# Kernel tuning notes

Measured on AMD Instinct MI355X. Metric: run time of the kernel, lower is better.

The kernel has to match this reference:

```python
import jax, jax.numpy as jnp
import numpy as np

DIVERSITY_RATE = 0.5


def setup_inputs() -> dict:
    key = jax.random.key(0)
    k1, k2 = jax.random.split(key)
    # model log-probabilities at current step: (bsz, beam, vocab)
    lprobs = jax.nn.log_softmax(
        jax.random.normal(k1, (128, 5, 50257), dtype=jnp.float32), axis=-1
    )
    # historical hypothesis scores: (bsz, beam, step)
    scores = jax.random.normal(k2, (128, 5, 10), dtype=jnp.float32)
    return {"lprobs": lprobs, "scores": scores, "step": 10}


def reference(lprobs, scores, step):
    bsz, beam_size, vocab_size = lprobs.shape
    k = min(beam_size * 2, beam_size * vocab_size - 1)  # = 10 here

    # step > 0 path: accumulate running score of each hypothesis
    lp = lprobs + scores[:, :, step - 1][:, :, None]  # (bsz, beam, vocab)

    # 1/ per-beam top-k over vocab (vectorized over all beams at once)
    s, idx = jax.lax.top_k(lp, k)  # (bsz, beam, k); idx already < vocab (fmod no-op)

    # 2/,3/ intra-sibling ordering -> rank penalty (rank r gets r*rate)
    sibling_score = jnp.arange(1, k + 1, dtype=lp.dtype) * DIVERSITY_RATE  # (k,)
    s = s - sibling_score  # broadcast over (bsz, beam, k)

    # 4/ final top-k over all beam*k candidates
    indices = idx.reshape(bsz, beam_size * k)
    final_scores, flat_pos = jax.lax.top_k(s.reshape(bsz, beam_size * k), k)
    final_beams = flat_pos // k  # which input beam each winner came from
    final_indices = jnp.take_along_axis(indices, flat_pos, axis=1)  # vocab ids

    return final_scores, final_indices, final_beams
```

## Files before the change

### kernel.cpp

```cpp
#include <hip/hip_runtime.h>
#include <hip/hip_bf16.h>
#include <math.h>
#include <stdint.h>


#define BS    256
#define KK    10
#define BEAM  5
#define CS    7168
#define NSLOT 7
#define CAP   1024
#define FCAP  2048

typedef unsigned long long u64;

__device__ __forceinline__ uint32_t ford(float x) {
    uint32_t u = __float_as_uint(x);
    return (u & 0x80000000u) ? ~u : (u | 0x80000000u);
}
__device__ __forceinline__ float funord(uint32_t u) {
    return __uint_as_float((u & 0x80000000u) ? (u & 0x7fffffffu) : ~u);
}

__device__ __forceinline__ void insert10(u64 (&key)[KK], u64 k) {
    if (k > key[KK - 1]) {
#pragma unroll
        for (int j = KK - 1; j >= 1; --j)
            key[j] = (k > key[j - 1]) ? key[j - 1] : ((k > key[j]) ? k : key[j]);
        if (k > key[0]) key[0] = k;
    }
}

__global__ __launch_bounds__(BS) void dss_chunk_topk(
    const float* __restrict__ lprobs,
    const float* __restrict__ scores,
    const int*   __restrict__ step_ptr,
    int vocab, int sdim, int nc,
    u64* __restrict__ ws_keys)
{
    const int chunk = blockIdx.x;
    const int row   = blockIdx.y;
    const int tid   = threadIdx.x;
    const int lane  = tid & 63;
    const int step  = step_ptr[0];
    const float bias = scores[(size_t)row * sdim + (step - 1)];

    const int c0 = chunk * CS;
    int len = vocab - c0; if (len > CS) len = CS;
    const float* cp = lprobs + (size_t)row * vocab + c0;

    __shared__ u64  cand[CAP];
    __shared__ int  s_cnt;

    int pre = (4 - (int)(((uintptr_t)cp >> 2) & 3)) & 3;
    if (pre > len) pre = len;
    const float4* g4 = (const float4*)(cp + pre);
    const int nvec = (len - pre) >> 2;
    const int done = pre + 4 * nvec;
    const int rem  = len - done;

    float4 v[NSLOT];
    float m = -INFINITY;
#pragma unroll
    for (int i = 0; i < NSLOT; ++i) {
        int idx = tid + (i << 8);
        if (idx < nvec) {
            float4 x = g4[idx];
            x.x += bias; x.y += bias; x.z += bias; x.w += bias;
            v[i] = x;
            m = fmaxf(m, fmaxf(fmaxf(x.x, x.y), fmaxf(x.z, x.w)));
        } else {
            v[i].x = -INFINITY; v[i].y = -INFINITY; v[i].z = -INFINITY; v[i].w = -INFINITY;
        }
    }
    float xv = -INFINITY; int xi = -1;
    if (tid < pre)                        { xi = tid;            xv = cp[xi] + bias; }
    else if (tid >= 4 && tid < 4 + rem)   { xi = done + tid - 4; xv = cp[xi] + bias; }
    m = fmaxf(m, xv);

    if (tid == 0) s_cnt = 0;

    int r = 0;
    const int mb = __float_as_int(m);
    for (int j = 0; j < 64; ++j) {
        float vj = __int_as_float(__builtin_amdgcn_readlane(mb, j));
        r += (vj > m || (vj == m && j < lane)) ? 1 : 0;
    }
    u64 msk = __ballot(r == 9);
    int src = __ffsll((long long)msk) - 1;
    const float tau = __int_as_float(__builtin_amdgcn_readlane(mb, src));

    __syncthreads();

    auto app = [&](float x, int j) {
        if (j < len) {
            int p = atomicAdd(&s_cnt, 1);
            if (p < CAP) cand[p] = ((u64)ford(x) << 32) | (uint32_t)~(c0 + j);
        }
    };
#pragma unroll
    for (int i = 0; i < NSLOT; ++i) {
        int base = pre + ((tid + (i << 8)) << 2);
        if (v[i].x >= tau) app(v[i].x, base + 0);
        if (v[i].y >= tau) app(v[i].y, base + 1);
        if (v[i].z >= tau) app(v[i].z, base + 2);
        if (v[i].w >= tau) app(v[i].w, base + 3);
    }
    if (xi >= 0 && xv >= tau) app(xv, xi);
    __syncthreads();

    int n = s_cnt; if (n > CAP) n = CAP;
    u64* outp = ws_keys + ((size_t)row * nc + chunk) * KK;
    for (int t = tid; t < n; t += BS) {
        u64 k = cand[t];
        int rk = 0;
        for (int j = 0; j < n; ++j) rk += (cand[j] > k) ? 1 : 0;
        if (rk < KK) outp[rk] = k;
    }
}

__global__ __launch_bounds__(BS) void dss_row_topk(
    const float* __restrict__ lprobs,
    const float* __restrict__ scores,
    const int*   __restrict__ step_ptr,
    int vocab, int sdim,
    u64* __restrict__ ws_keys)
{
    const int row = blockIdx.x;
    const int tid = threadIdx.x;
    const int step = step_ptr[0];
    const float bias = scores[(size_t)row * sdim + (step - 1)];
    const float* rp = lprobs + (size_t)row * vocab;

    __shared__ u64  cand[FCAP];
    __shared__ u64  skey[BS * KK];
    __shared__ int  cnt;
    __shared__ float sh_tau;

    int pre = (4 - (int)(((uintptr_t)rp >> 2) & 3)) & 3;
    if (pre > vocab) pre = vocab;
    const float4* p4 = (const float4*)(rp + pre);
    const int nvec = (vocab - pre) >> 2;
    const int done = pre + 4 * nvec;
    const int rem  = vocab - done;

    float m = -INFINITY;
    if (tid < pre) m = rp[tid] + bias;
    for (int t = tid; t < nvec; t += BS) {
        float4 x = p4[t];
        m = fmaxf(m, fmaxf(fmaxf(x.x + bias, x.y + bias), fmaxf(x.z + bias, x.w + bias)));
    }
    if (tid < rem) m = fmaxf(m, rp[done + tid] + bias);

    skey[tid * KK] = ((u64)ford(m) << 32) | (uint32_t)~tid;
#pragma unroll
    for (int j = 1; j < KK; ++j) skey[tid * KK + j] = 0;
    if (tid == 0) cnt = 0;
    __syncthreads();
    for (int off = BS / 2; off >= 1; off >>= 1) {
        if (tid < off) {
            const int pa = tid * KK, pb = (tid + off) * KK;
            u64 mk[KK]; int ia = 0, ib = 0;
#pragma unroll
            for (int j = 0; j < KK; ++j) {
                u64 ka = skey[pa + ia], kb = skey[pb + ib];
                bool tA = (ka >= kb); mk[j] = tA ? ka : kb;
                if (tA) ++ia; else ++ib;
            }
#pragma unroll
            for (int j = 0; j < KK; ++j) skey[pa + j] = mk[j];
        }
        __syncthreads();
    }
    if (tid == 0) sh_tau = funord((uint32_t)(skey[9] >> 32));
    __syncthreads();
    const float tau = sh_tau;

    auto app = [&](float x, int i) {
        if (x >= tau) {
            int p = atomicAdd(&cnt, 1);
            if (p < FCAP) cand[p] = ((u64)ford(x) << 32) | (uint32_t)~i;
        }
    };
    if (tid < pre) app(rp[tid] + bias, tid);
    for (int t = tid; t < nvec; t += BS) {
        float4 x = p4[t];
        int base = pre + 4 * t;
        app(x.x + bias, base + 0); app(x.y + bias, base + 1);
        app(x.z + bias, base + 2); app(x.w + bias, base + 3);
    }
    if (tid < rem) app(rp[done + tid] + bias, done + tid);
    __syncthreads();

    const int n = (cnt < FCAP) ? cnt : FCAP;
    {
        u64 key[KK];
#pragma unroll
        for (int j = 0; j < KK; ++j) key[j] = 0;
        for (int i = tid; i < n; i += BS) insert10(key, cand[i]);
#pragma unroll
        for (int j = 0; j < KK; ++j) skey[tid * KK + j] = key[j];
    }
    __syncthreads();
    for (int off = BS / 2; off >= 1; off >>= 1) {
        if (tid < off) {
            const int pa = tid * KK, pb = (tid + off) * KK;
            u64 mk[KK]; int ia = 0, ib = 0;
#pragma unroll
            for (int j = 0; j < KK; ++j) {
                u64 ka = skey[pa + ia], kb = skey[pb + ib];
                bool tA = (ka >= kb); mk[j] = tA ? ka : kb;
                if (tA) ++ia; else ++ib;
            }
#pragma unroll
            for (int j = 0; j < KK; ++j) skey[pa + j] = mk[j];
        }
        __syncthreads();
    }
    if (tid < KK) ws_keys[(size_t)row * KK + tid] = skey[tid];
}

__global__ __launch_bounds__(512) void dss_final(
    const u64* __restrict__ ws_keys,
    float* __restrict__ out, int bsz, int nc)
{
    const int b = blockIdx.x;
    const int t = threadIdx.x;
    const int NC  = nc * KK;
    const int tot = BEAM * NC;

    __shared__ u64  kbuf[BEAM * KK * 8];
    __shared__ float pen[BEAM * KK];
    __shared__ int   pidx[BEAM * KK];

    for (int i = t; i < tot; i += 512) kbuf[i] = ws_keys[(size_t)b * tot + i];
    __syncthreads();

    if (t < tot) {
        int beam = t / NC;
        u64 k = kbuf[t];
        const u64* kb = kbuf + beam * NC;
        int r = 0;
        for (int j = 0; j < NC; ++j) r += (kb[j] > k) ? 1 : 0;
        if (r < KK) {
            pen [beam * KK + r] = funord((uint32_t)(k >> 32)) - 0.5f * (float)(r + 1);
            pidx[beam * KK + r] = (int)~(uint32_t)k;
        }
    }
    __syncthreads();

    if (t < BEAM * KK) {
        float p = pen[t];
        int r = 0;
        for (int j = 0; j < BEAM * KK; ++j) {
            float q = pen[j];
            r += (q > p || (q == p && j < t)) ? 1 : 0;
        }
        if (r < KK) {
            out[              b * KK + r] = p;
            out[(size_t)bsz * KK     + b * KK + r] = (float)pidx[t];
            out[(size_t)2 * bsz * KK + b * KK + r] = (float)(t / KK);
        }
    }
}

extern "C" void kernel_launch(void* const* d_in, const int* in_sizes, int n_in,
                              void* d_out, int out_size, void* d_ws, size_t ws_size,
                              hipStream_t stream)
{
    const float* lprobs = (const float*)d_in[0];
    const float* scores = (const float*)d_in[1];
    const int*   step   = (const int*)d_in[2];

    const int bsz   = 128;
    const int rows  = bsz * BEAM;
    const int vocab = in_sizes[0] / rows;
    const int sdim  = in_sizes[1] / rows;

    u64* ws_keys = (u64*)d_ws;

    int nc = (vocab + CS - 1) / CS;
    if (nc > 8) nc = 8;
    if (ws_size < (size_t)rows * nc * KK * sizeof(u64)) nc = 1;

    if (nc > 1) {
        dss_chunk_topk<<<dim3(nc, rows), BS, 0, stream>>>(
            lprobs, scores, step, vocab, sdim, nc, ws_keys);
    } else {
        dss_row_topk<<<rows, BS, 0, stream>>>(lprobs, scores, step, vocab, sdim, ws_keys);
    }
    dss_final<<<bsz, 512, 0, stream>>>(ws_keys, (float*)d_out, bsz, nc);
}
```

Measured before the change: 200.2 us.

## Fuse chunk top-k and final merge via last-block counter; retune chunk size

```diff
diff --git a/kernel.cpp b/kernel.cpp
--- a/kernel.cpp
+++ b/kernel.cpp
@@ -7,8 +7,8 @@
 #define BS    256
 #define KK    10
 #define BEAM  5
-#define CS    7168
-#define NSLOT 7
+#define NSLOT 6
+#define CS    (BS * NSLOT * 4)
 #define CAP   1024
 #define FCAP  2048
 
@@ -31,15 +31,18 @@
     }
 }
 
-__global__ __launch_bounds__(BS) void dss_chunk_topk(
+__global__ __launch_bounds__(BS, 8) void dss_fused(
     const float* __restrict__ lprobs,
     const float* __restrict__ scores,
     const int*   __restrict__ step_ptr,
-    int vocab, int sdim, int nc,
-    u64* __restrict__ ws_keys)
+    int vocab, int sdim, int nc, int bsz,
+    int* __restrict__ counters,
+    u64* __restrict__ ws_keys,
+    float* __restrict__ out)
 {
     const int chunk = blockIdx.x;
     const int row   = blockIdx.y;
+    const int bb    = row / BEAM;
     const int tid   = threadIdx.x;
     const int lane  = tid & 63;
     const int step  = step_ptr[0];
@@ -49,8 +52,13 @@
     int len = vocab - c0; if (len > CS) len = CS;
     const float* cp = lprobs + (size_t)row * vocab + c0;
 
-    __shared__ u64  cand[CAP];
-    __shared__ int  s_cnt;
+    __shared__ u64   cand[CAP];
+    __shared__ float sgrp[16];
+    __shared__ int   s_cnt;
+    __shared__ int   s_last;
+    __shared__ u64   kbuf[BEAM * KK * 9];
+    __shared__ float pen [BEAM * KK];
+    __shared__ int   pidx[BEAM * KK];
 
     int pre = (4 - (int)(((uintptr_t)cp >> 2) & 3)) & 3;
     if (pre > len) pre = len;
@@ -80,17 +88,14 @@
 
     if (tid == 0) s_cnt = 0;
 
-    int r = 0;
-    const int mb = __float_as_int(m);
-    for (int j = 0; j < 64; ++j) {
-        float vj = __int_as_float(__builtin_amdgcn_readlane(mb, j));
-        r += (vj > m || (vj == m && j < lane)) ? 1 : 0;
-    }
-    u64 msk = __ballot(r == 9);
-    int src = __ffsll((long long)msk) - 1;
-    const float tau = __int_as_float(__builtin_amdgcn_readlane(mb, src));
-
-    __syncthreads();
+    float gm = m;
+#pragma unroll
+    for (int o = 1; o <= 8; o <<= 1) gm = fmaxf(gm, __shfl_xor(gm, o));
+    if ((lane & 15) == 0) sgrp[(tid >> 6) * 4 + (lane >> 4)] = gm;
+    __syncthreads();
+    float tau = sgrp[0];
+#pragma unroll
+    for (int g = 1; g < 16; ++g) tau = fminf(tau, sgrp[g]);
 
     auto app = [&](float x, int j) {
         if (j < len) {
@@ -111,11 +116,55 @@
 
     int n = s_cnt; if (n > CAP) n = CAP;
     u64* outp = ws_keys + ((size_t)row * nc + chunk) * KK;
-    for (int t = tid; t < n; t += BS) {
-        u64 k = cand[t];
+    for (int t2 = tid; t2 < n; t2 += BS) {
+        u64 k = cand[t2];
         int rk = 0;
         for (int j = 0; j < n; ++j) rk += (cand[j] > k) ? 1 : 0;
-        if (rk < KK) outp[rk] = k;
+        if (rk < KK)
+            __hip_atomic_store(&outp[rk], k, __ATOMIC_RELEASE, __HIP_MEMORY_SCOPE_AGENT);
+    }
+    __syncthreads();
+
+    if (tid == 0) {
+        int old = __hip_atomic_fetch_add(&counters[bb], 1, __ATOMIC_ACQ_REL,
+                                         __HIP_MEMORY_SCOPE_AGENT);
+        s_last = (old == BEAM * nc - 1) ? 1 : 0;
+    }
+    __syncthreads();
+    if (!s_last) return;
+
+    const int NC  = nc * KK;
+    const int tot = BEAM * NC;
+    const u64* src = ws_keys + (size_t)bb * tot;
+    for (int i = tid; i < tot; i += BS)
+        kbuf[i] = __hip_atomic_load(&src[i], __ATOMIC_RELAXED, __HIP_MEMORY_SCOPE_AGENT);
+    __syncthreads();
+
+    for (int i = tid; i < tot; i += BS) {
+        int beam = i / NC;
+        u64 k = kbuf[i];
+        const u64* kb = kbuf + beam * NC;
+        int r = 0;
+        for (int j = 0; j < NC; ++j) r += (kb[j] > k) ? 1 : 0;
+        if (r < KK) {
+            pen [beam * KK + r] = funord((uint32_t)(k >> 32)) - 0.5f * (float)(r + 1);
+            pidx[beam * KK + r] = (int)~(uint32_t)k;
+        }
+    }
+    __syncthreads();
+
+    if (tid < BEAM * KK) {
+        float p = pen[tid];
+        int r = 0;
+        for (int j = 0; j < BEAM * KK; ++j) {
+            float q = pen[j];
+            r += (q > p || (q == p && j < tid)) ? 1 : 0;
+        }
+        if (r < KK) {
+            out[                       bb * KK + r] = p;
+            out[(size_t)bsz * KK     + bb * KK + r] = (float)pidx[tid];
+            out[(size_t)2 * bsz * KK + bb * KK + r] = (float)(tid / KK);
+        }
     }
 }
 
@@ -229,7 +278,7 @@
     const int NC  = nc * KK;
     const int tot = BEAM * NC;
 
-    __shared__ u64  kbuf[BEAM * KK * 8];
+    __shared__ u64  kbuf[BEAM * KK * 9];
     __shared__ float pen[BEAM * KK];
     __shared__ int   pidx[BEAM * KK];
 
@@ -277,17 +326,20 @@
     const int vocab = in_sizes[0] / rows;
     const int sdim  = in_sizes[1] / rows;
 
-    u64* ws_keys = (u64*)d_ws;
-
     int nc = (vocab + CS - 1) / CS;
-    if (nc > 8) nc = 8;
-    if (ws_size < (size_t)rows * nc * KK * sizeof(u64)) nc = 1;
-
-    if (nc > 1) {
-        dss_chunk_topk<<<dim3(nc, rows), BS, 0, stream>>>(
-            lprobs, scores, step, vocab, sdim, nc, ws_keys);
+    if (nc > 9) nc = 9;
+
+    const size_t need = 1024 + (size_t)rows * nc * KK * sizeof(u64);
+    if (nc > 1 && ws_size >= need) {
+        int* counters = (int*)d_ws;
+        u64* ws_keys  = (u64*)((char*)d_ws + 1024);
+        hipMemsetAsync(d_ws, 0, 1024, stream);
+        dss_fused<<<dim3(nc, rows), BS, 0, stream>>>(
+            lprobs, scores, step, vocab, sdim, nc, bsz,
+            counters, ws_keys, (float*)d_out);
     } else {
+        u64* ws_keys = (u64*)d_ws;
         dss_row_topk<<<rows, BS, 0, stream>>>(lprobs, scores, step, vocab, sdim, ws_keys);
-    }
-    dss_final<<<bsz, 512, 0, stream>>>(ws_keys, (float*)d_out, bsz, nc);
-}
+        dss_final<<<bsz, 512, 0, stream>>>(ws_keys, (float*)d_out, bsz, 1);
+    }
+}
```

Result: slower. 544.0 us (+171.7%).
